# Performance work log

Measured on AMD Instinct MI355X. Metric: run time of the kernel, lower is better.

The kernel has to match this reference:

```python
import jax, jax.numpy as jnp
from jax import lax
import numpy as np

SHAPE = (64, 64, 64)  # spatial grid (D, H, W)
N_PTS = 100000        # active voxels
KPAD = (1, 2, 2)      # 'same' padding for (3,5,5) kernel


def _conv(x, w, pad):
    # x: [B,D,H,W,C], w: [kd,kh,kw,Cin,Cout]
    return lax.conv_general_dilated(
        x, w, window_strides=(1, 1, 1),
        padding=[(p, p) for p in pad],
        dimension_numbers=('NDHWC', 'DHWIO', 'NDHWC'))


def _sparse_maxpool2(x, mask):
    # spconv SparseMaxPool3d(2,2): output active where any input in 2x2x2
    # window is active; value = max over active inputs only.
    neg = jnp.float32(-1e30)
    xm = jnp.where(mask > 0, x, neg)
    win = (1, 2, 2, 2, 1)
    y = lax.reduce_window(xm, neg, lax.max, win, win, 'VALID')
    m2 = lax.reduce_window(mask, jnp.float32(0), lax.max, win, win, 'VALID')
    return jnp.where(m2 > 0, y, 0.0), m2


def setup_inputs() -> dict:
    rng = np.random.default_rng(0)
    D, H, W = SHAPE
    lin = rng.choice(D * H * W, size=N_PTS, replace=False)  # unique voxels
    z = lin // (H * W)
    y = (lin // W) % H
    x = lin % W
    coors = np.stack([np.zeros(N_PTS, np.int32), z, y, x], 1).astype(np.int32)

    key = jax.random.key(0)
    ks = jax.random.split(key, 16)
    feats = jax.random.normal(ks[0], (N_PTS, 3), jnp.float32)

    dims = [(3, 64), (64, 64), (64, 96), (96, 96), (96, 128), (128, 128),
            (128, 160), (160, 160), (160, 192), (192, 192), (192, 224),
            (224, 224), (224, 256), (256, 256)]
    inp = {'features': feats, 'coors': jnp.asarray(coors), 'batch_size': 1}
    for i, (ci, co) in enumerate(dims):
        scale = 1.0 / np.sqrt(ci * 75.0)  # 75 = 3*5*5 kernel taps
        inp[f'w{i}'] = jax.random.normal(ks[i + 1], (3, 5, 5, ci, co),
                                         jnp.float32) * scale
    return inp


def reference(features, coors, batch_size,
              w0, w1, w2, w3, w4, w5, w6, w7, w8, w9, w10, w11, w12, w13):
    # Densify the sparse tensor: inactive voxels are exactly zero, so a dense
    # conv followed by masking to the active set reproduces submanifold conv.
    b, z, y, x = coors[:, 0], coors[:, 1], coors[:, 2], coors[:, 3]
    dense = jnp.zeros((1,) + SHAPE + (3,), jnp.float32).at[b, z, y, x].set(features)
    mask = jnp.zeros((1,) + SHAPE + (1,), jnp.float32).at[b, z, y, x].set(1.0)

    ws = [w0, w1, w2, w3, w4, w5, w6, w7, w8, w9, w10, w11]
    h = dense
    wi = 0
    for _lvl in range(6):  # 6 (subm, subm, pool2) stages
        h = _conv(h, ws[wi], KPAD) * mask; wi += 1
        h = _conv(h, ws[wi], KPAD) * mask; wi += 1
        h, mask = _sparse_maxpool2(h, mask)

    # SparseConv3d(224,256,(3,5,5),padding=(1,2,2)): output active set is the
    # dilation of the input active set by the kernel footprint.
    m2 = lax.reduce_window(mask, jnp.float32(0), lax.max,
                           (1, 3, 5, 5, 1), (1, 1, 1, 1, 1),
                           [(0, 0), (1, 1), (2, 2), (2, 2), (0, 0)])
    h = _conv(h, w12, KPAD) * m2
    mask = m2
    # final SubMConv3d(256,256)
    h = _conv(h, w13, KPAD) * mask
    return h  # [1,1,1,1,256]
```

## Files before the change

kernel.cpp:

```cpp
#include <hip/hip_runtime.h>
#include <hip/hip_bf16.h>
#include <cstdint>

typedef __attribute__((ext_vector_type(8))) short bf16x8;
typedef __attribute__((ext_vector_type(4))) float f32x4;

__device__ __forceinline__ unsigned short f2bf_hi(float v) {
    unsigned u = __float_as_uint(v);
    u = u + 0x7fffu + ((u >> 16) & 1u);
    return (unsigned short)(u >> 16);
}
__device__ __forceinline__ float bf2f(unsigned short h) {
    return __uint_as_float(((unsigned)h) << 16);
}

__global__ void scatter_kernel(const float* __restrict__ feats,
                               const int* __restrict__ coors,
                               float* __restrict__ dense,
                               float* __restrict__ mask, int n)
{
    int i = blockIdx.x * blockDim.x + threadIdx.x;
    if (i >= n) return;
    const int z = coors[i * 4 + 1];
    const int y = coors[i * 4 + 2];
    const int x = coors[i * 4 + 3];
    const size_t s = (size_t)((z * 64 + y) * 64 + x);
    dense[s * 3 + 0] = feats[i * 3 + 0];
    dense[s * 3 + 1] = feats[i * 3 + 1];
    dense[s * 3 + 2] = feats[i * 3 + 2];
    mask[s] = 1.f;
}

__global__ void wprep_kernel(const float* __restrict__ w,
                             unsigned short* __restrict__ wv, int CI, int CO)
{
    const int total = 75 * CI * CO;
    const int stride = gridDim.x * blockDim.x;
    for (int i = blockIdx.x * blockDim.x + threadIdx.x; i < total; i += stride) {
        const int tap = i / (CI * CO);
        const int r = i - tap * CI * CO;
        const int ci = r / CO;
        const int co = r - ci * CO;
        const size_t o = ((size_t)(tap * (CI / 8) + (ci >> 3)) * CO + co) * 8 + (ci & 7);
        wv[o] = f2bf_hi(w[i]);
    }
}

__global__ void wprep2_kernel(const float* __restrict__ w,
                              unsigned short* __restrict__ wv, int CI, int CO)
{
    const int total = 75 * CI * CO;
    const int stride = gridDim.x * blockDim.x;
    for (int i = blockIdx.x * blockDim.x + threadIdx.x; i < total; i += stride) {
        const int tap = i / (CI * CO);
        const int r = i - tap * CI * CO;
        const int ci = r / CO;
        const int co = r - ci * CO;
        const float v = w[i];
        const unsigned short h = f2bf_hi(v);
        const unsigned short l = f2bf_hi(v - bf2f(h));
        const size_t o = ((size_t)(tap * (CI / 8) + (ci >> 3)) * CO + co) * 16 + (ci & 7);
        wv[o] = h; wv[o + 8] = l;
    }
}

__global__ __launch_bounds__(256)
void conv1_kernel(const float* __restrict__ in, const float* __restrict__ w,
                  const float* __restrict__ mask, unsigned short* __restrict__ ob)
{
    constexpr int S = 64, SP = 68;
    __shared__ float lds[15][3][SP];

    const int bid = blockIdx.y * S + blockIdx.x;
    const int wg = (bid & 7) * (S * S / 8) + (bid >> 3);
    const int y = wg & 63, z = wg >> 6;
    const int t = threadIdx.x;

    for (int idx = t; idx < 15 * 3 * SP; idx += 256) {
        const int r = idx / (3 * SP);
        const int rem = idx - r * 3 * SP;
        const int ci = rem / SP;
        const int x = rem - ci * SP;
        const int kz = r / 5, ky = r - kz * 5;
        const int zz = z + kz - 1, yy = y + ky - 2, xi = x - 2;
        float v = 0.f;
        if ((unsigned)zz < (unsigned)S && (unsigned)yy < (unsigned)S && (unsigned)xi < (unsigned)S)
            v = in[(size_t)((zz * S + yy) * S + xi) * 3 + ci];
        lds[r][ci][x] = v;
    }
    __syncthreads();

    const int co = t & 63, xs = t >> 6;
    float acc[16];
#pragma unroll
    for (int i = 0; i < 16; ++i) acc[i] = 0.f;

#pragma unroll 1
    for (int r = 0; r < 15; ++r) {
#pragma unroll
        for (int ci = 0; ci < 3; ++ci) {
            float inv[20];
#pragma unroll
            for (int j = 0; j < 5; ++j)
                *(float4*)&inv[j * 4] = *(const float4*)&lds[r][ci][xs * 16 + j * 4];
            const float* wp = w + (size_t)(r * 15 + ci) * 64 + co;
#pragma unroll
            for (int kx = 0; kx < 5; ++kx) {
                const float wv = wp[kx * 192];
#pragma unroll
                for (int i = 0; i < 16; ++i) acc[i] += inv[i + kx] * wv;
            }
        }
    }

    const size_t vb = (size_t)(z * S + y) * S;
#pragma unroll
    for (int i = 0; i < 16; ++i) {
        const int x = xs * 16 + i;
        const float keep = (mask[vb + x] > 0.f) ? 1.f : 0.f;
        ob[(vb + x) * 64 + co] = f2bf_hi(acc[i] * keep);
    }
}

template<int CIN, int COUT, int S, int YB, int YG, int WN, int NG, int OMODE>
__global__ __launch_bounds__(YG * NG * 64)
void mfma_conv7(const unsigned short* __restrict__ ab,
                const unsigned short* __restrict__ wv,
                const float* __restrict__ mask, float* __restrict__ outf,
                unsigned short* __restrict__ outb)
{
    constexpr int SP = S + 4;
    constexpr int MX = S / 16;
    constexpr int KC = CIN / 32;
    constexpr int KC4 = CIN / 8;
    constexpr int RS = (KC4 <= 8) ? 8 : 16;
    constexpr int PLANE = SP * RS;
    constexpr int NLR = SP * KC4;
    constexpr int NL = 2 * NLR;
    constexpr int NW = YG * NG;
    constexpr int NT = NW * 64;
    constexpr int SREG = (NL + NT - 1) / NT;
    constexpr int YBW = YB / YG;
    constexpr int NYB = S / YB;
    constexpr int JP = (YB + 4) / 2;
    constexpr int NP = 3 * JP;
    static_assert(COUT / 16 == WN * NG, "geometry");
    static_assert((YB + 4) % 2 == 0, "YB even");

    __shared__ unsigned short lds[2 * 2 * PLANE * 8];

    const int bid = blockIdx.y * NYB + blockIdx.x;
    constexpr int NWG = NYB * S;
    const int wg = (bid & 7) * (NWG / 8) + (bid >> 3);
    const int yb = wg % NYB, z = wg / NYB;
    const int y0 = yb * YB;

    const int t = threadIdx.x;
    const int lane = t & 63;
    const int wave = t >> 6;
    const int waveN = wave % NG;
    const int waveY = wave / NG;
    const int col = lane & 15;
    const int ci8 = lane >> 4;

    f32x4 acc[YBW][MX][WN];
    const f32x4 vzero = {0.f, 0.f, 0.f, 0.f};
#pragma unroll
    for (int q = 0; q < YBW; ++q)
#pragma unroll
        for (int m = 0; m < MX; ++m)
#pragma unroll
            for (int n = 0; n < WN; ++n) acc[q][m][n] = vzero;

    uint4 reg[SREG];

    auto issue = [&](int ph) {
        const int kz = ph / JP, jp = ph - kz * JP;
        const int zz = z + kz - 1;
        const bool zv = ((unsigned)zz < (unsigned)S);
#pragma unroll
        for (int i = 0; i < SREG; ++i) {
            const int L = i * NT + t;
            uint4 v = {0u, 0u, 0u, 0u};
            if (L < NL) {
                const int jr = L / NLR;
                const int l2 = L - jr * NLR;
                const int x = l2 / KC4;
                const int c3 = l2 - x * KC4;
                const int xi = x - 2;
                const int yy = y0 + jp * 2 + jr - 2;
                if (zv && (unsigned)yy < (unsigned)S && (unsigned)xi < (unsigned)S)
                    v = *(const uint4*)(ab + (size_t)((zz * S + yy) * S + xi) * CIN + c3 * 8);
            }
            reg[i] = v;
        }
    };
    auto store = [&](int pl) {
#pragma unroll
        for (int i = 0; i < SREG; ++i) {
            const int L = i * NT + t;
            if (L < NL) {
                const int jr = L / NLR;
                const int l2 = L - jr * NLR;
                const int x = l2 / KC4;
                const int c3 = l2 - x * KC4;
                const int p = x * RS + (c3 ^ (x & 7));
                *(uint4*)&lds[((pl * 2 + jr) * PLANE + p) * 8] = reg[i];
            }
        }
    };

    issue(0);
    store(0);
    if (NP > 1) issue(1);
    __syncthreads();

    int cur = 0;
#pragma unroll 1
    for (int ph = 0; ph < NP; ++ph) {
        const int kz = ph / JP, jp = ph - kz * JP;
        const int zz = z + kz - 1;
        if ((unsigned)zz < (unsigned)S) {
#pragma unroll
            for (int jr = 0; jr < 2; ++jr) {
                const int j = jp * 2 + jr;
                const int yy = y0 + j - 2;
                if ((unsigned)yy >= (unsigned)S) continue;
                const unsigned short* plane = lds + (cur * 2 + jr) * PLANE * 8;

                bool vq[YBW];
                int tapb[YBW];
#pragma unroll
                for (int ql = 0; ql < YBW; ++ql) {
                    const int q = waveY * YBW + ql;
                    const int ky = j - q;
                    vq[ql] = (ky >= 0 && ky <= 4);
                    tapb[ql] = (kz * 5 + (vq[ql] ? ky : 0)) * 5;
                }

                bf16x8 wA[YBW][KC][WN], wB[YBW][KC][WN];
                auto wload = [&](bf16x8 (&wb)[YBW][KC][WN], int kx) {
#pragma unroll
                    for (int ql = 0; ql < YBW; ++ql) if (vq[ql]) {
                        const int tap = tapb[ql] + kx;
#pragma unroll
                        for (int kc = 0; kc < KC; ++kc) {
                            const int c3 = kc * 4 + ci8;
#pragma unroll
                            for (int n = 0; n < WN; ++n) {
                                const int co = (waveN * WN + n) * 16 + col;
                                wb[ql][kc][n] = *(const bf16x8*)(wv + ((size_t)(tap * KC4 + c3) * COUT + co) * 8);
                            }
                        }
                    }
                };
                auto wmfma = [&](bf16x8 (&wb)[YBW][KC][WN], bf16x8 (&a)[KC][MX]) {
#pragma unroll
                    for (int ql = 0; ql < YBW; ++ql) if (vq[ql])
#pragma unroll
                        for (int kc = 0; kc < KC; ++kc)
#pragma unroll
                            for (int m = 0; m < MX; ++m)
#pragma unroll
                                for (int n = 0; n < WN; ++n)
                                    acc[ql][m][n] = __builtin_amdgcn_mfma_f32_16x16x32_bf16(a[kc][m], wb[ql][kc][n], acc[ql][m][n], 0, 0, 0);
                };

                wload(wA, 0);
                __builtin_amdgcn_s_setprio(1);
#pragma unroll
                for (int kx = 0; kx < 5; ++kx) {
                    bf16x8 a[KC][MX];
#pragma unroll
                    for (int kc = 0; kc < KC; ++kc) {
                        const int c3 = kc * 4 + ci8;
#pragma unroll
                        for (int m = 0; m < MX; ++m) {
                            const int x = m * 16 + col + kx;
                            const int p = x * RS + (c3 ^ (x & 7));
                            a[kc][m] = *(const bf16x8*)&plane[p * 8];
                        }
                    }
                    if ((kx & 1) == 0) {
                        if (kx + 1 < 5) wload(wB, kx + 1);
                        wmfma(wA, a);
                    } else {
                        if (kx + 1 < 5) wload(wA, kx + 1);
                        wmfma(wB, a);
                    }
                }
                __builtin_amdgcn_s_setprio(0);
            }
        }
        if (ph + 1 < NP) store(cur ^ 1);
        if (ph + 2 < NP) issue(ph + 2);
        __syncthreads();
        cur ^= 1;
    }

    const int rq = lane >> 4;
#pragma unroll
    for (int ql = 0; ql < YBW; ++ql) {
        const int y = y0 + waveY * YBW + ql;
        const size_t vb = (size_t)(z * S + y) * S;
#pragma unroll
        for (int m = 0; m < MX; ++m) {
            const int xb = m * 16 + rq * 4;
#pragma unroll
            for (int r = 0; r < 4; ++r) {
                const int x = xb + r;
                const float keep = (mask[vb + x] > 0.f) ? 1.f : 0.f;
#pragma unroll
                for (int n = 0; n < WN; ++n) {
                    const int co = (waveN * WN + n) * 16 + col;
                    const float v = acc[ql][m][n][r] * keep;
                    if (OMODE == 0) outf[(vb + x) * COUT + co] = v;
                    else            outb[(vb + x) * COUT + co] = f2bf_hi(v);
                }
            }
        }
    }
}

template<int CIN, int COUT, int S, int YB, int YG, int WN, int NG, int OMODE>
__global__ __launch_bounds__(YG * NG * 64)
void mfma_conv6(const unsigned short* __restrict__ ab,
                const unsigned short* __restrict__ wv,
                const float* __restrict__ mask, float* __restrict__ outf,
                unsigned short* __restrict__ outb)
{
    constexpr int SP = S + 4;
    constexpr int MX = S / 16;
    constexpr int KC = CIN / 32;
    constexpr int KC4 = CIN / 8;
    constexpr int RS = (KC4 <= 8) ? 8 : 16;
    constexpr int PLANE = SP * RS;
    constexpr int NL = SP * KC4;
    constexpr int NW = YG * NG;
    constexpr int NT = NW * 64;
    constexpr int SREG = (NL + NT - 1) / NT;
    constexpr int YBW = YB / YG;
    constexpr int NYB = S / YB;
    constexpr int NP = 3 * (YB + 4);
    static_assert(COUT / 16 == WN * NG, "geometry");

    __shared__ unsigned short lds[2 * PLANE * 8];

    const int bid = blockIdx.y * NYB + blockIdx.x;
    constexpr int NWG = NYB * S;
    const int wg = (bid & 7) * (NWG / 8) + (bid >> 3);
    const int yb = wg % NYB, z = wg / NYB;
    const int y0 = yb * YB;

    const int t = threadIdx.x;
    const int lane = t & 63;
    const int wave = t >> 6;
    const int waveN = wave % NG;
    const int waveY = wave / NG;
    const int col = lane & 15;
    const int ci8 = lane >> 4;

    f32x4 acc[YBW][MX][WN];
    const f32x4 vzero = {0.f, 0.f, 0.f, 0.f};
#pragma unroll
    for (int q = 0; q < YBW; ++q)
#pragma unroll
        for (int m = 0; m < MX; ++m)
#pragma unroll
            for (int n = 0; n < WN; ++n) acc[q][m][n] = vzero;

    uint4 reg[SREG];

    auto issue = [&](int ph) {
        const int kz = ph / (YB + 4), j = ph - kz * (YB + 4);
        const int zz = z + kz - 1, yy = y0 + j - 2;
        const bool rv = ((unsigned)zz < (unsigned)S) && ((unsigned)yy < (unsigned)S);
        const size_t rowbase = rv ? (size_t)((zz * S + yy) * S) * CIN : 0;
#pragma unroll
        for (int i = 0; i < SREG; ++i) {
            const int L = i * NT + t;
            uint4 v = {0u, 0u, 0u, 0u};
            if (L < NL) {
                const int x = L / KC4;
                const int c3 = L - x * KC4;
                const int xi = x - 2;
                if (rv && (unsigned)xi < (unsigned)S)
                    v = *(const uint4*)(ab + rowbase + (size_t)xi * CIN + c3 * 8);
            }
            reg[i] = v;
        }
    };
    auto store = [&](int pl) {
#pragma unroll
        for (int i = 0; i < SREG; ++i) {
            const int L = i * NT + t;
            if (L < NL) {
                const int x = L / KC4;
                const int c3 = L - x * KC4;
                const int p = x * RS + (c3 ^ (x & 7));
                *(uint4*)&lds[(pl * PLANE + p) * 8] = reg[i];
            }
        }
    };

    issue(0);
    store(0);
    if (NP > 1) issue(1);
    __syncthreads();

    int cur = 0;
#pragma unroll 1
    for (int ph = 0; ph < NP; ++ph) {
        const int kz = ph / (YB + 4), j = ph - kz * (YB + 4);
        const int zz = z + kz - 1, yy = y0 + j - 2;
        if (((unsigned)zz < (unsigned)S) && ((unsigned)yy < (unsigned)S)) {
            const unsigned short* plane = lds + cur * PLANE * 8;

            bool vq[YBW];
            int tapb[YBW];
#pragma unroll
            for (int ql = 0; ql < YBW; ++ql) {
                const int q = waveY * YBW + ql;
                const int ky = j - q;
                vq[ql] = (ky >= 0 && ky <= 4);
                tapb[ql] = (kz * 5 + (vq[ql] ? ky : 0)) * 5;
            }

            bf16x8 wA[YBW][KC][WN], wB[YBW][KC][WN];
            auto wload = [&](bf16x8 (&wb)[YBW][KC][WN], int kx) {
#pragma unroll
                for (int ql = 0; ql < YBW; ++ql) if (vq[ql]) {
                    const int tap = tapb[ql] + kx;
#pragma unroll
                    for (int kc = 0; kc < KC; ++kc) {
                        const int c3 = kc * 4 + ci8;
#pragma unroll
                        for (int n = 0; n < WN; ++n) {
                            const int co = (waveN * WN + n) * 16 + col;
                            wb[ql][kc][n] = *(const bf16x8*)(wv + ((size_t)(tap * KC4 + c3) * COUT + co) * 8);
                        }
                    }
                }
            };
            auto wmfma = [&](bf16x8 (&wb)[YBW][KC][WN], bf16x8 (&a)[KC][MX]) {
#pragma unroll
                for (int ql = 0; ql < YBW; ++ql) if (vq[ql])
#pragma unroll
                    for (int kc = 0; kc < KC; ++kc)
#pragma unroll
                        for (int m = 0; m < MX; ++m)
#pragma unroll
                            for (int n = 0; n < WN; ++n)
                                acc[ql][m][n] = __builtin_amdgcn_mfma_f32_16x16x32_bf16(a[kc][m], wb[ql][kc][n], acc[ql][m][n], 0, 0, 0);
            };

            wload(wA, 0);
            __builtin_amdgcn_s_setprio(1);
#pragma unroll
            for (int kx = 0; kx < 5; ++kx) {
                bf16x8 a[KC][MX];
#pragma unroll
                for (int kc = 0; kc < KC; ++kc) {
                    const int c3 = kc * 4 + ci8;
#pragma unroll
                    for (int m = 0; m < MX; ++m) {
                        const int x = m * 16 + col + kx;
                        const int p = x * RS + (c3 ^ (x & 7));
                        a[kc][m] = *(const bf16x8*)&plane[p * 8];
                    }
                }
                if ((kx & 1) == 0) {
                    if (kx + 1 < 5) wload(wB, kx + 1);
                    wmfma(wA, a);
                } else {
                    if (kx + 1 < 5) wload(wA, kx + 1);
                    wmfma(wB, a);
                }
            }
            __builtin_amdgcn_s_setprio(0);
        }
        if (ph + 1 < NP) store(cur ^ 1);
        if (ph + 2 < NP) issue(ph + 2);
        __syncthreads();
        cur ^= 1;
    }

    const int rq = lane >> 4;
#pragma unroll
    for (int ql = 0; ql < YBW; ++ql) {
        const int y = y0 + waveY * YBW + ql;
        const size_t vb = (size_t)(z * S + y) * S;
#pragma unroll
        for (int m = 0; m < MX; ++m) {
            const int xb = m * 16 + rq * 4;
#pragma unroll
            for (int r = 0; r < 4; ++r) {
                const int x = xb + r;
                const float keep = (mask[vb + x] > 0.f) ? 1.f : 0.f;
#pragma unroll
                for (int n = 0; n < WN; ++n) {
                    const int co = (waveN * WN + n) * 16 + col;
                    const float v = acc[ql][m][n][r] * keep;
                    if (OMODE == 0) outf[(vb + x) * COUT + co] = v;
                    else            outb[(vb + x) * COUT + co] = f2bf_hi(v);
                }
            }
        }
    }
}

template<int CIN, int COUT, int S, int WM, int WN, int MG, int NG, int OMODE>
__global__ __launch_bounds__(MG * NG * 64)
void mfma_conv3c(const unsigned short* __restrict__ ab,
                 const unsigned short* __restrict__ wv,
                 const float* __restrict__ mask, float* __restrict__ outf,
                 unsigned short* __restrict__ outb)
{
    constexpr int SP = S + 4;
    constexpr int KC = CIN / 32;
    constexpr int KC4 = CIN / 8;
    constexpr int RS = (KC4 <= 8) ? 8 : 16;
    constexpr int PLANE = SP * RS;
    constexpr int NL = SP * KC4;
    constexpr int NT = MG * NG * 64;
    constexpr int SREG = (NL + NT - 1) / NT;
    static_assert(S / 16 == WM * MG && COUT / 16 == WN * NG, "geometry");

    __shared__ unsigned short lds[2 * PLANE * 8];

    const int bid = blockIdx.y * S + blockIdx.x;
    const int wg = (bid & 7) * (S * S / 8) + (bid >> 3);
    const int y = wg % S, z = wg / S;

    const int t = threadIdx.x;
    const int lane = t & 63;
    const int wave = t >> 6;
    const int waveM = wave % MG;
    const int waveN = wave / MG;
    const int col = lane & 15;
    const int ci8 = lane >> 4;

    f32x4 acc[WM][WN];
    const f32x4 vzero = {0.f, 0.f, 0.f, 0.f};
#pragma unroll
    for (int m = 0; m < WM; ++m)
#pragma unroll
        for (int n = 0; n < WN; ++n) acc[m][n] = vzero;

    uint4 reg[SREG];

    auto issue = [&](int kzy) {
        const int kz = kzy / 5, ky = kzy - kz * 5;
        const int zz = z + kz - 1, yy = y + ky - 2;
        const bool rv = ((unsigned)zz < (unsigned)S) && ((unsigned)yy < (unsigned)S);
        const size_t rowbase = rv ? (size_t)((zz * S + yy) * S) * CIN : 0;
#pragma unroll
        for (int i = 0; i < SREG; ++i) {
            const int L = i * NT + t;
            uint4 v = {0u, 0u, 0u, 0u};
            if (L < NL) {
                const int x = L / KC4;
                const int c3 = L - x * KC4;
                const int xi = x - 2;
                if (rv && (unsigned)xi < (unsigned)S)
                    v = *(const uint4*)(ab + rowbase + (size_t)xi * CIN + c3 * 8);
            }
            reg[i] = v;
        }
    };
    auto store = [&](int pl) {
#pragma unroll
        for (int i = 0; i < SREG; ++i) {
            const int L = i * NT + t;
            if (L < NL) {
                const int x = L / KC4;
                const int c3 = L - x * KC4;
                const int p = x * RS + (c3 ^ (x & 7));
                *(uint4*)&lds[(pl * PLANE + p) * 8] = reg[i];
            }
        }
    };

    issue(0);
    store(0);
    issue(1);
    __syncthreads();

    int cur = 0;
#pragma unroll 1
    for (int kzy = 0; kzy < 15; ++kzy) {
        const int kz = kzy / 5, ky = kzy - kz * 5;
        const int zz = z + kz - 1, yy = y + ky - 2;
        if (((unsigned)zz < (unsigned)S) && ((unsigned)yy < (unsigned)S)) {
            const unsigned short* plane = lds + cur * PLANE * 8;

            bf16x8 wA[KC][WN], wB[KC][WN];
            auto wload = [&](bf16x8 (&wb)[KC][WN], int kx) {
                const int tap = kzy * 5 + kx;
#pragma unroll
                for (int kc = 0; kc < KC; ++kc) {
                    const int c3 = kc * 4 + ci8;
#pragma unroll
                    for (int n = 0; n < WN; ++n) {
                        const int co = (waveN * WN + n) * 16 + col;
                        wb[kc][n] = *(const bf16x8*)(wv + ((size_t)(tap * KC4 + c3) * COUT + co) * 8);
                    }
                }
            };
            auto wmfma = [&](bf16x8 (&wb)[KC][WN], bf16x8 (&a)[KC][WM]) {
#pragma unroll
                for (int kc = 0; kc < KC; ++kc)
#pragma unroll
                    for (int m = 0; m < WM; ++m)
#pragma unroll
                        for (int n = 0; n < WN; ++n)
                            acc[m][n] = __builtin_amdgcn_mfma_f32_16x16x32_bf16(a[kc][m], wb[kc][n], acc[m][n], 0, 0, 0);
            };

            wload(wA, 0);
            __builtin_amdgcn_s_setprio(1);
#pragma unroll
            for (int kx = 0; kx < 5; ++kx) {
                bf16x8 a[KC][WM];
#pragma unroll
                for (int kc = 0; kc < KC; ++kc) {
                    const int c3 = kc * 4 + ci8;
#pragma unroll
                    for (int m = 0; m < WM; ++m) {
                        const int x = (waveM * WM + m) * 16 + col + kx;
                        const int p = x * RS + (c3 ^ (x & 7));
                        a[kc][m] = *(const bf16x8*)&plane[p * 8];
                    }
                }
                if ((kx & 1) == 0) {
                    if (kx + 1 < 5) wload(wB, kx + 1);
                    wmfma(wA, a);
                } else {
                    if (kx + 1 < 5) wload(wA, kx + 1);
                    wmfma(wB, a);
                }
            }
            __builtin_amdgcn_s_setprio(0);
        }
        if (kzy + 1 < 15) store(cur ^ 1);
        if (kzy + 2 < 15) issue(kzy + 2);
        __syncthreads();
        cur ^= 1;
    }

    const int rq = lane >> 4;
    const size_t vb = (size_t)(z * S + y) * S;
#pragma unroll
    for (int m = 0; m < WM; ++m) {
        const int xb = (waveM * WM + m) * 16 + rq * 4;
#pragma unroll
        for (int r = 0; r < 4; ++r) {
            const int x = xb + r;
            const float keep = (mask[vb + x] > 0.f) ? 1.f : 0.f;
#pragma unroll
            for (int n = 0; n < WN; ++n) {
                const int co = (waveN * WN + n) * 16 + col;
                const float v = acc[m][n][r] * keep;
                if (OMODE == 0) outf[(vb + x) * COUT + co] = v;
                else            outb[(vb + x) * COUT + co] = f2bf_hi(v);
            }
        }
    }
}

template<int CIN, int COUT, int S, int NW>
__global__ __launch_bounds__(NW * 64)
void dgemm2_kernel(const unsigned short* __restrict__ inb,
                   const unsigned short* __restrict__ wv,
                   const float* __restrict__ mask,
                   unsigned short* __restrict__ outb)
{
    constexpr int M = S * S * S;
    constexpr int KC = CIN / 32;
    constexpr int KC4 = CIN / 8;
    __shared__ f32x4 part[NW][64];

    const int t = threadIdx.x;
    const int lane = t & 63;
    const int w = t >> 6;
    const int col = lane & 15;
    const int g = lane >> 4;

    const int va = blockIdx.x * 16 + col;
    const bool av = (va < M);
    const int az = (va / (S * S)) % S;
    const int ay = (va / S) % S;
    const int ax = va % S;
    const int co = blockIdx.y * 16 + col;

    f32x4 acc0 = {0.f, 0.f, 0.f, 0.f};
    f32x4 acc1 = {0.f, 0.f, 0.f, 0.f};

#pragma unroll 2
    for (int tap = w; tap < 75; tap += NW) {
        const int dz = tap / 25 - 1;
        const int dy = (tap / 5) % 5 - 2;
        const int dx = tap % 5 - 2;
        const int zz = az + dz, yy = ay + dy, xx = ax + dx;
        const bool valid = av && ((unsigned)zz < (unsigned)S) &&
                           ((unsigned)yy < (unsigned)S) && ((unsigned)xx < (unsigned)S);
        const size_t abase = valid ? (size_t)((zz * S + yy) * S + xx) * CIN : 0;
#pragma unroll
        for (int kc = 0; kc < KC; ++kc) {
            const int c3 = kc * 4 + g;
            bf16x8 a = {0, 0, 0, 0, 0, 0, 0, 0};
            if (valid) a = *(const bf16x8*)(inb + abase + c3 * 8);
            const unsigned short* wp = wv + ((size_t)(tap * KC4 + c3) * COUT + co) * 16;
            bf16x8 wh = *(const bf16x8*)wp;
            bf16x8 wl = *(const bf16x8*)(wp + 8);
            acc0 = __builtin_amdgcn_mfma_f32_16x16x32_bf16(a, wh, acc0, 0, 0, 0);
            acc1 = __builtin_amdgcn_mfma_f32_16x16x32_bf16(a, wl, acc1, 0, 0, 0);
        }
    }

    part[w][lane] = acc0 + acc1;
    __syncthreads();

    if (w == 0) {
        f32x4 s = part[0][lane];
#pragma unroll
        for (int i = 1; i < NW; ++i) s += part[i][lane];
#pragma unroll
        for (int r = 0; r < 4; ++r) {
            const int v = blockIdx.x * 16 + g * 4 + r;
            if (v < M) {
                const float keep = (mask[v] > 0.f) ? 1.f : 0.f;
                outb[(size_t)v * COUT + co] = f2bf_hi(s[r] * keep);
            }
        }
    }
}

__global__ void pool_bf8_kernel(const unsigned short* __restrict__ inb,
                                const float* __restrict__ mi,
                                unsigned short* __restrict__ outb,
                                float* __restrict__ mo, int S, int C)
{
    const int So = S >> 1;
    const int C8 = C >> 3;
    const long long total = (long long)So * So * So * C8;
    for (long long i = blockIdx.x * (long long)blockDim.x + threadIdx.x; i < total;
         i += (long long)gridDim.x * blockDim.x) {
        const int c8 = (int)(i % C8);
        const long long s = i / C8;
        const int xo = (int)(s % So);
        const int yo = (int)((s / So) % So);
        const int zo = (int)(s / ((long long)So * So));
        float best[8];
#pragma unroll
        for (int k = 0; k < 8; ++k) best[k] = -1e30f;
        float m2 = 0.f;
        for (int dz = 0; dz < 2; ++dz)
            for (int dy = 0; dy < 2; ++dy)
                for (int dx = 0; dx < 2; ++dx) {
                    const int zi = zo * 2 + dz, yi = yo * 2 + dy, xi = xo * 2 + dx;
                    const float m = mi[(zi * S + yi) * S + xi];
                    if (m > 0.f) {
                        m2 = 1.f;
                        const unsigned short* p =
                            inb + ((size_t)((zi * S + yi) * S + xi) * C8 + c8) * 8;
                        uint4 v = *(const uint4*)p;
                        const unsigned short* vs = (const unsigned short*)&v;
#pragma unroll
                        for (int k = 0; k < 8; ++k) best[k] = fmaxf(best[k], bf2f(vs[k]));
                    }
                }
        uint4 o;
        unsigned short* os = (unsigned short*)&o;
#pragma unroll
        for (int k = 0; k < 8; ++k) os[k] = f2bf_hi((m2 > 0.f) ? best[k] : 0.f);
        *(uint4*)(outb + i * 8) = o;
        if (c8 == 0) mo[s] = m2;
    }
}

__global__ __launch_bounds__(256)
void final_kernel(const unsigned short* __restrict__ h, const float* __restrict__ mask,
                  const float* __restrict__ w12, const float* __restrict__ w13,
                  float* __restrict__ out)
{
    __shared__ float o1[256];
    const int co = threadIdx.x;
    const float m = (mask[0] > 0.f) ? 1.f : 0.f;
    float a = 0.f;
    for (int ci = 0; ci < 224; ++ci)
        a += bf2f(h[ci]) * w12[(size_t)(37 * 224 + ci) * 256 + co];
    o1[co] = a * m;
    __syncthreads();
    float b = 0.f;
    for (int ci = 0; ci < 256; ++ci)
        b += o1[ci] * w13[(size_t)(37 * 256 + ci) * 256 + co];
    out[co] = b * m;
}

static void pool_bf8(const unsigned short* inb, const float* mi,
                     unsigned short* outb, float* mo, int S, int C, hipStream_t stream)
{
    const long long total = (long long)(S / 2) * (S / 2) * (S / 2) * (C / 8);
    long long grid = (total + 255) / 256;
    if (grid > 4096) grid = 4096;
    if (grid < 1) grid = 1;
    pool_bf8_kernel<<<(int)grid, 256, 0, stream>>>(inb, mi, outb, mo, S, C);
}

#define WOFF0 0
#define WOFF1 307200
#define WOFF2 768000
#define WOFF3 1459200
#define WOFF4 2380800
#define DOFF6 0
#define DOFF7 3072000
#define DOFF8 6912000
#define DOFF9 11520000
#define DOFF10 17049600
#define DOFF11 23500800

extern "C" void kernel_launch(void* const* d_in, const int* in_sizes, int n_in,
                              void* d_out, int out_size, void* d_ws, size_t ws_size,
                              hipStream_t stream)
{
    const float* feats = (const float*)d_in[0];
    const int*   coors = (const int*)d_in[1];
    const float* w[14];
    for (int i = 0; i < 14; ++i) w[i] = (const float*)d_in[3 + i];
    float* outp = (float*)d_out;

    float* dense0 = (float*)d_ws;
    float* mA = dense0 + 786432;
    float* mB = mA + 262144;
    unsigned short* ab = (unsigned short*)(mB + 262144);
    unsigned short* bb = ab + 16777216;
    unsigned short* wvp = bb + 16777216;
    unsigned short* wdp = wvp + 3609600;

    const int npts = in_sizes[0] / 3;

    wprep_kernel<<<2048, 256, 0, stream>>>(w[1], wvp + WOFF0, 64, 64);
    wprep_kernel<<<2048, 256, 0, stream>>>(w[2], wvp + WOFF1, 64, 96);
    wprep_kernel<<<2048, 256, 0, stream>>>(w[3], wvp + WOFF2, 96, 96);
    wprep_kernel<<<2048, 256, 0, stream>>>(w[4], wvp + WOFF3, 96, 128);
    wprep_kernel<<<2048, 256, 0, stream>>>(w[5], wvp + WOFF4, 128, 128);
    wprep2_kernel<<<2048, 256, 0, stream>>>(w[6], wdp + DOFF6, 128, 160);
    wprep2_kernel<<<2048, 256, 0, stream>>>(w[7], wdp + DOFF7, 160, 160);
    wprep2_kernel<<<2048, 256, 0, stream>>>(w[8], wdp + DOFF8, 160, 192);
    wprep2_kernel<<<2048, 256, 0, stream>>>(w[9], wdp + DOFF9, 192, 192);
    wprep2_kernel<<<2048, 256, 0, stream>>>(w[10], wdp + DOFF10, 192, 224);
    wprep2_kernel<<<2048, 256, 0, stream>>>(w[11], wdp + DOFF11, 224, 224);

    hipMemsetAsync(dense0, 0, (size_t)786432 * sizeof(float), stream);
    hipMemsetAsync(mA, 0, (size_t)262144 * sizeof(float), stream);
    scatter_kernel<<<(npts + 255) / 256, 256, 0, stream>>>(feats, coors, dense0, mA, npts);

    conv1_kernel<<<dim3(64, 64), 256, 0, stream>>>(dense0, w[0], mA, ab);
    mfma_conv7<64, 64, 64, 4, 2, 2, 2, 1><<<dim3(16, 64), 256, 0, stream>>>(
        ab, wvp + WOFF0, mA, nullptr, bb);
    pool_bf8(bb, mA, ab, mB, 64, 64, stream);
    mfma_conv6<64, 96, 32, 2, 1, 2, 3, 1><<<dim3(16, 32), 192, 0, stream>>>(
        ab, wvp + WOFF1, mB, nullptr, bb);
    mfma_conv6<96, 96, 32, 2, 1, 2, 3, 1><<<dim3(16, 32), 192, 0, stream>>>(
        bb, wvp + WOFF2, mB, nullptr, ab);
    pool_bf8(ab, mB, bb, mA, 32, 96, stream);
    mfma_conv3c<96, 128, 16, 1, 2, 1, 4, 1><<<dim3(16, 16), 256, 0, stream>>>(
        bb, wvp + WOFF3, mA, nullptr, ab);
    mfma_conv3c<128, 128, 16, 1, 2, 1, 4, 1><<<dim3(16, 16), 256, 0, stream>>>(
        ab, wvp + WOFF4, mA, nullptr, bb);
    pool_bf8(bb, mA, ab, mB, 16, 128, stream);
    dgemm2_kernel<128, 160, 8, 4><<<dim3(32, 10), 256, 0, stream>>>(ab, wdp + DOFF6, mB, bb);
    dgemm2_kernel<160, 160, 8, 4><<<dim3(32, 10), 256, 0, stream>>>(bb, wdp + DOFF7, mB, ab);
    pool_bf8(ab, mB, bb, mA, 8, 160, stream);
    dgemm2_kernel<160, 192, 4, 8><<<dim3(4, 12), 512, 0, stream>>>(bb, wdp + DOFF8, mA, ab);
    dgemm2_kernel<192, 192, 4, 8><<<dim3(4, 12), 512, 0, stream>>>(ab, wdp + DOFF9, mA, bb);
    pool_bf8(bb, mA, ab, mB, 4, 192, stream);
    dgemm2_kernel<192, 224, 2, 8><<<dim3(1, 14), 512, 0, stream>>>(ab, wdp + DOFF10, mB, bb);
    dgemm2_kernel<224, 224, 2, 8><<<dim3(1, 14), 512, 0, stream>>>(bb, wdp + DOFF11, mB, ab);
    pool_bf8(ab, mB, bb, mA, 2, 224, stream);
    final_kernel<<<1, 256, 0, stream>>>(bb, mA, w[12], w[13], outp);
}
```

Baseline: 783.2 us.

## Rewrite first 3-to-64 channel conv as bf16 MFMA im2col GEMM

The first sparse conv layer (3 input channels) moves from a scalar FP32 FMA kernel to an MFMA kernel. It flattens the 225 taps×channels into a K dimension padded to 256 and gathers im2col rows from LDS. The dense input grid is now stored as bf16, and weights are split into hi/lo bf16 pairs so accuracy stays near fp32 at the cost of two MFMAs per step. This targets the scalar-ALU-bound first layer, but the input is now quantized to bf16 and the LDS gather uses scattered short loads.

```diff
diff --git a/kernel.cpp b/kernel.cpp
--- a/kernel.cpp
+++ b/kernel.cpp
@@ -16,7 +16,7 @@
 
 __global__ void scatter_kernel(const float* __restrict__ feats,
                                const int* __restrict__ coors,
-                               float* __restrict__ dense,
+                               unsigned short* __restrict__ dense,
                                float* __restrict__ mask, int n)
 {
     int i = blockIdx.x * blockDim.x + threadIdx.x;
@@ -25,9 +25,9 @@
     const int y = coors[i * 4 + 2];
     const int x = coors[i * 4 + 3];
     const size_t s = (size_t)((z * 64 + y) * 64 + x);
-    dense[s * 3 + 0] = feats[i * 3 + 0];
-    dense[s * 3 + 1] = feats[i * 3 + 1];
-    dense[s * 3 + 2] = feats[i * 3 + 2];
+    dense[s * 3 + 0] = f2bf_hi(feats[i * 3 + 0]);
+    dense[s * 3 + 1] = f2bf_hi(feats[i * 3 + 1]);
+    dense[s * 3 + 2] = f2bf_hi(feats[i * 3 + 2]);
     mask[s] = 1.f;
 }
 
@@ -64,61 +64,98 @@
     }
 }
 
+__global__ void wprep1_kernel(const float* __restrict__ w,
+                              unsigned short* __restrict__ wv1)
+{
+    const int i = blockIdx.x * blockDim.x + threadIdx.x;
+    if (i >= 256 * 64) return;
+    const int k = i >> 6, co = i & 63;
+    unsigned short h = 0, l = 0;
+    if (k < 225) {
+        const float v = w[k * 64 + co];
+        h = f2bf_hi(v);
+        l = f2bf_hi(v - bf2f(h));
+    }
+    const size_t o = (size_t)(k >> 3) * 1024 + co * 16 + (k & 7);
+    wv1[o] = h; wv1[o + 8] = l;
+}
+
 __global__ __launch_bounds__(256)
-void conv1_kernel(const float* __restrict__ in, const float* __restrict__ w,
-                  const float* __restrict__ mask, unsigned short* __restrict__ ob)
-{
-    constexpr int S = 64, SP = 68;
-    __shared__ float lds[15][3][SP];
+void conv1m_kernel(const unsigned short* __restrict__ in,
+                   const unsigned short* __restrict__ wv1,
+                   const float* __restrict__ mask, unsigned short* __restrict__ ob)
+{
+    constexpr int S = 64;
+    constexpr int RW = 204;
+    constexpr int RP = 208;
+    __shared__ unsigned short lds[15 * RP];
 
     const int bid = blockIdx.y * S + blockIdx.x;
     const int wg = (bid & 7) * (S * S / 8) + (bid >> 3);
     const int y = wg & 63, z = wg >> 6;
     const int t = threadIdx.x;
 
-    for (int idx = t; idx < 15 * 3 * SP; idx += 256) {
-        const int r = idx / (3 * SP);
-        const int rem = idx - r * 3 * SP;
-        const int ci = rem / SP;
-        const int x = rem - ci * SP;
+    for (int idx = t; idx < 15 * RW; idx += 256) {
+        const int r = idx / RW;
+        const int q = idx - r * RW;
+        const int xp = q / 3, ci = q - xp * 3;
         const int kz = r / 5, ky = r - kz * 5;
-        const int zz = z + kz - 1, yy = y + ky - 2, xi = x - 2;
-        float v = 0.f;
+        const int zz = z + kz - 1, yy = y + ky - 2, xi = xp - 2;
+        unsigned short v = 0;
         if ((unsigned)zz < (unsigned)S && (unsigned)yy < (unsigned)S && (unsigned)xi < (unsigned)S)
             v = in[(size_t)((zz * S + yy) * S + xi) * 3 + ci];
-        lds[r][ci][x] = v;
+        lds[r * RP + q] = v;
     }
     __syncthreads();
 
-    const int co = t & 63, xs = t >> 6;
-    float acc[16];
-#pragma unroll
-    for (int i = 0; i < 16; ++i) acc[i] = 0.f;
-
-#pragma unroll 1
-    for (int r = 0; r < 15; ++r) {
-#pragma unroll
-        for (int ci = 0; ci < 3; ++ci) {
-            float inv[20];
-#pragma unroll
-            for (int j = 0; j < 5; ++j)
-                *(float4*)&inv[j * 4] = *(const float4*)&lds[r][ci][xs * 16 + j * 4];
-            const float* wp = w + (size_t)(r * 15 + ci) * 64 + co;
-#pragma unroll
-            for (int kx = 0; kx < 5; ++kx) {
-                const float wv = wp[kx * 192];
-#pragma unroll
-                for (int i = 0; i < 16; ++i) acc[i] += inv[i + kx] * wv;
-            }
-        }
-    }
-
+    const int lane = t & 63;
+    const int xf = t >> 6;
+    const int col = lane & 15;
+    const int ci8 = lane >> 4;
+
+    f32x4 acc[4];
+    const f32x4 vzero = {0.f, 0.f, 0.f, 0.f};
+#pragma unroll
+    for (int n = 0; n < 4; ++n) acc[n] = vzero;
+
+    const int abase = (xf * 16 + col) * 3;
+
+#pragma unroll
+    for (int kc = 0; kc < 8; ++kc) {
+        unsigned short av[8];
+#pragma unroll
+        for (int e = 0; e < 8; ++e) {
+            int k = kc * 32 + ci8 * 8 + e;
+            if (k > 224) k = 224;
+            const int tap = k / 3, ci = k - 3 * tap;
+            const int kzy = tap / 5, kx = tap - kzy * 5;
+            av[e] = lds[kzy * RP + abase + kx * 3 + ci];
+        }
+        bf16x8 a;
+#pragma unroll
+        for (int e = 0; e < 8; ++e) ((unsigned short*)&a)[e] = av[e];
+
+#pragma unroll
+        for (int n = 0; n < 4; ++n) {
+            const unsigned short* wp = wv1 + (size_t)(kc * 4 + ci8) * 1024 + (n * 16 + col) * 16;
+            bf16x8 wh = *(const bf16x8*)wp;
+            bf16x8 wl = *(const bf16x8*)(wp + 8);
+            acc[n] = __builtin_amdgcn_mfma_f32_16x16x32_bf16(a, wh, acc[n], 0, 0, 0);
+            acc[n] = __builtin_amdgcn_mfma_f32_16x16x32_bf16(a, wl, acc[n], 0, 0, 0);
+        }
+    }
+
+    const int rq = lane >> 4;
     const size_t vb = (size_t)(z * S + y) * S;
 #pragma unroll
-    for (int i = 0; i < 16; ++i) {
-        const int x = xs * 16 + i;
+    for (int r = 0; r < 4; ++r) {
+        const int x = xf * 16 + rq * 4 + r;
         const float keep = (mask[vb + x] > 0.f) ? 1.f : 0.f;
-        ob[(vb + x) * 64 + co] = f2bf_hi(acc[i] * keep);
+#pragma unroll
+        for (int n = 0; n < 4; ++n) {
+            const int co = n * 16 + col;
+            ob[(vb + x) * 64 + co] = f2bf_hi(acc[n][r] * keep);
+        }
     }
 }
 
@@ -830,16 +867,18 @@
     for (int i = 0; i < 14; ++i) w[i] = (const float*)d_in[3 + i];
     float* outp = (float*)d_out;
 
-    float* dense0 = (float*)d_ws;
-    float* mA = dense0 + 786432;
+    unsigned short* dense0 = (unsigned short*)d_ws;
+    float* mA = (float*)d_ws + 786432;
     float* mB = mA + 262144;
     unsigned short* ab = (unsigned short*)(mB + 262144);
     unsigned short* bb = ab + 16777216;
     unsigned short* wvp = bb + 16777216;
     unsigned short* wdp = wvp + 3609600;
+    unsigned short* wv1 = wdp + 31104000;
 
     const int npts = in_sizes[0] / 3;
 
+    wprep1_kernel<<<64, 256, 0, stream>>>(w[0], wv1);
     wprep_kernel<<<2048, 256, 0, stream>>>(w[1], wvp + WOFF0, 64, 64);
     wprep_kernel<<<2048, 256, 0, stream>>>(w[2], wvp + WOFF1, 64, 96);
     wprep_kernel<<<2048, 256, 0, stream>>>(w[3], wvp + WOFF2, 96, 96);
@@ -852,11 +891,11 @@
     wprep2_kernel<<<2048, 256, 0, stream>>>(w[10], wdp + DOFF10, 192, 224);
     wprep2_kernel<<<2048, 256, 0, stream>>>(w[11], wdp + DOFF11, 224, 224);
 
-    hipMemsetAsync(dense0, 0, (size_t)786432 * sizeof(float), stream);
+    hipMemsetAsync(dense0, 0, (size_t)786432 * sizeof(unsigned short), stream);
     hipMemsetAsync(mA, 0, (size_t)262144 * sizeof(float), stream);
     scatter_kernel<<<(npts + 255) / 256, 256, 0, stream>>>(feats, coors, dense0, mA, npts);
 
-    conv1_kernel<<<dim3(64, 64), 256, 0, stream>>>(dense0, w[0], mA, ab);
+    conv1m_kernel<<<dim3(64, 64), 256, 0, stream>>>(dense0, wv1, mA, ab);
     mfma_conv7<64, 64, 64, 4, 2, 2, 2, 1><<<dim3(16, 64), 256, 0, stream>>>(
         ab, wvp + WOFF0, mA, nullptr, bb);
     pool_bf8(bb, mA, ab, mB, 64, 64, stream);
```

After: 725.1 us. -7.4%, faster.
